# Performance work log

Measured on AMD Instinct MI355X. Metric: run time of the kernel, lower is better.

## Reference

```python
import jax, jax.numpy as jnp
import numpy as np

N_HEADS = 16
MAX_REL = 64  # max_relative_pos_len


def setup_inputs() -> dict:
    key = jax.random.key(0)
    ks = jax.random.split(key, 8)
    B, S, D = 2, 2048, 1024
    d = D // N_HEADS
    sc = 0.02
    return {
        "hidden_states": jax.random.normal(ks[0], (B, S, D), jnp.float32),
        "attention_mask": jnp.zeros((B, 1, 1, S), jnp.float32),
        "Wq": jax.random.normal(ks[1], (D, D), jnp.float32) * sc,
        "bq": jnp.zeros((D,), jnp.float32),
        "Wk": jax.random.normal(ks[2], (D, D), jnp.float32) * sc,
        "bk": jnp.zeros((D,), jnp.float32),
        "Wv": jax.random.normal(ks[3], (D, D), jnp.float32) * sc,
        "bv": jnp.zeros((D,), jnp.float32),
        "emb_k": jax.random.normal(ks[4], (2 * MAX_REL + 1, d), jnp.float32) * sc,
        "emb_v": jax.random.normal(ks[5], (2 * MAX_REL + 1, d), jnp.float32) * sc,
    }


def reference(hidden_states, attention_mask, Wq, bq, Wk, bk, Wv, bv, emb_k, emb_v):
    B, S, D = hidden_states.shape
    H = N_HEADS
    d = D // H
    scale = 1.0 / jnp.sqrt(jnp.asarray(d, hidden_states.dtype))

    def heads(x):  # [B,S,D] -> [B,H,S,d]
        return x.reshape(B, S, H, d).transpose(0, 2, 1, 3)

    q = heads(hidden_states @ Wq + bq)
    k = heads(hidden_states @ Wk + bk)
    v = heads(hidden_states @ Wv + bv)

    # relative position indices, clamped: [S_q, S_k]
    rel_idx = jnp.clip(jnp.arange(S)[:, None] - jnp.arange(S)[None, :], -MAX_REL, MAX_REL) + MAX_REL
    rel_k = emb_k[rel_idx]  # [S, S, d]

    # content scores + relative-key bias, both scaled by 1/sqrt(d)
    scores = (jnp.einsum('bhqd,bhkd->bhqk', q, k)
              + jnp.einsum('bhqd,qkd->bhqk', q, rel_k)) * scale
    scores = scores + attention_mask
    probs = jax.nn.softmax(scores, axis=-1)  # dropout is identity at p=0

    rel_v = emb_v[rel_idx]  # [S, S, d]
    ctx = (jnp.einsum('bhqk,bhkd->bhqd', probs, v)
           + jnp.einsum('bhqk,qkd->bhqd', probs, rel_v))
    return ctx.transpose(0, 2, 1, 3).reshape(B, S, D)
```

## Files before the change

kernel.cpp:

```cpp
#include <hip/hip_runtime.h>
#include <stdint.h>

typedef unsigned short u16;
typedef __attribute__((ext_vector_type(8))) short short8;
typedef __attribute__((ext_vector_type(4))) float f32x4;
typedef __attribute__((ext_vector_type(4))) unsigned short u16x4;

#define S_LEN 2048
#define NH 16
#define DMODEL 1024
#define NR 129
#define LOG2E 1.44269504f

#define MFMA(a,b,c) __builtin_amdgcn_mfma_f32_16x16x32_bf16((a),(b),(c),0,0,0)

__device__ __forceinline__ u16 f2bf(float f){
  uint32_t u = __float_as_uint(f);
  u += 0x7fff + ((u >> 16) & 1);
  return (u16)(u >> 16);
}
__device__ __forceinline__ float bf2f(u16 h){ return __uint_as_float(((uint32_t)h) << 16); }

__device__ __forceinline__ uint32_t cvtpk(float lo, float hi){
  uint32_t r;
  asm("v_cvt_pk_bf16_f32 %0, %1, %2" : "=v"(r) : "v"(lo), "v"(hi));
  return r;
}

__device__ __forceinline__ void gl_lds16(const u16* g, u16* l){
  __builtin_amdgcn_global_load_lds((const __attribute__((address_space(1))) void*)g,
                                   (__attribute__((address_space(3))) void*)l, 16, 0, 0);
}

__global__ __launch_bounds__(256) void k_prep(const float* __restrict__ X,
                                              const float* __restrict__ Wq, const float* __restrict__ Wk,
                                              const float* __restrict__ Wv, const float* __restrict__ Wemb,
                                              const float* __restrict__ mask,
                                              u16* __restrict__ Xb, u16* __restrict__ Wt,
                                              u16* __restrict__ Eb, float* __restrict__ maskL){
  const int bid = blockIdx.x, tid = threadIdx.x;
  if (bid < 4096){
    int i = bid * 256 + tid;
    const float4* xp = (const float4*)X;
    float4 v = xp[i];
    u16x4 o; o.x = f2bf(v.x); o.y = f2bf(v.y); o.z = f2bf(v.z); o.w = f2bf(v.w);
    *(u16x4*)(Xb + (size_t)i * 4) = o;
  } else if (bid < 4864){
    int b2 = bid - 4096;
    int z = b2 >> 8;
    const float* W = (z == 0) ? Wq : (z == 1) ? Wk : Wv;
    u16* Ot = Wt + (size_t)z * 1024 * 1024;
    __shared__ float t[64][65];
    int k0 = ((b2 >> 4) & 15) * 64, n0 = (b2 & 15) * 64;
    int c = tid & 63, r0 = (tid >> 6) * 16;
    #pragma unroll
    for (int i = 0; i < 16; ++i) t[r0 + i][c] = W[(size_t)(k0 + r0 + i) * 1024 + n0 + c];
    __syncthreads();
    #pragma unroll
    for (int i = 0; i < 16; ++i) Ot[(size_t)(n0 + r0 + i) * 1024 + k0 + c] = f2bf(t[c][r0 + i]);
  } else if (bid < 4900){
    int idx = (bid - 4864) * 256 + tid;
    if (idx < 144 * 64){
      int r = idx >> 6;
      Eb[idx] = (r < NR) ? f2bf(Wemb[idx]) : (u16)0;
    }
  } else {
    int idx = (bid - 4900) * 256 + tid;
    maskL[idx] = mask[idx] * LOG2E;
  }
}

__global__ __launch_bounds__(256) void k_qkv(const u16* __restrict__ Xb, const u16* __restrict__ Wt,
                                             const float* __restrict__ bq, const float* __restrict__ bk,
                                             const float* __restrict__ bv,
                                             u16* __restrict__ Qs, u16* __restrict__ Kb, u16* __restrict__ Vp){
  const int z = blockIdx.z;
  const u16* W = Wt + (size_t)z * 1024 * 1024;
  const float* bias = (z == 0) ? bq : (z == 1) ? bk : bv;
  const float vs = (z == 0) ? 0.125f * LOG2E : 1.0f;
  const int n0 = blockIdx.x * 128, m0 = blockIdx.y * 128;
  const int tid = threadIdx.x, w = tid >> 6, lane = tid & 63, l15 = lane & 15, quad = lane >> 4;
  const int wm = (w >> 1) * 64, wn = (w & 1) * 64;
  __shared__ __attribute__((aligned(16))) u16 As[128 * 32];
  __shared__ __attribute__((aligned(16))) u16 Bs[128 * 32];
  __shared__ __attribute__((aligned(16))) u16 Ts[64][136];
  f32x4 acc[4][4];
  #pragma unroll
  for (int i = 0; i < 4; ++i)
    #pragma unroll
    for (int j = 0; j < 4; ++j) acc[i][j] = (f32x4){0.f,0.f,0.f,0.f};

  const int rA = lane >> 2, cA = (lane & 3) * 8;
  const u16* aBase = Xb + (size_t)(m0 + w * 16 + rA) * 1024 + cA;
  const u16* bBase = W  + (size_t)(n0 + w * 16 + rA) * 1024 + cA;
  u16* aDst0 = As + (w * 16) * 32;  u16* aDst1 = As + (64 + w * 16) * 32;
  u16* bDst0 = Bs + (w * 16) * 32;  u16* bDst1 = Bs + (64 + w * 16) * 32;

  if (z == 2){
    for (int k0 = 0; k0 < 1024; k0 += 32){
      __syncthreads();
      gl_lds16(aBase + k0,             aDst0);
      gl_lds16(aBase + 64 * 1024 + k0, aDst1);
      gl_lds16(bBase + k0,             bDst0);
      gl_lds16(bBase + 64 * 1024 + k0, bDst1);
      __syncthreads();
      short8 af[4], bfr[4];
      #pragma unroll
      for (int f = 0; f < 4; ++f){
        af[f]  = *(const short8*)(As + (wm + f * 16 + l15) * 32 + quad * 8);
        bfr[f] = *(const short8*)(Bs + (wn + f * 16 + l15) * 32 + quad * 8);
      }
      #pragma unroll
      for (int i = 0; i < 4; ++i)
        #pragma unroll
        for (int j = 0; j < 4; ++j) acc[i][j] = MFMA(af[i], bfr[j], acc[i][j]);
    }
    const int hn0 = n0 >> 6;
    const int bb = m0 >> 11, sb = m0 & 2047;
    #pragma unroll
    for (int h2 = 0; h2 < 2; ++h2){
      __syncthreads();
      if ((w & 1) == h2){
        #pragma unroll
        for (int i = 0; i < 4; ++i){
          int sl0 = (w >> 1) * 64 + i * 16 + quad * 4;
          #pragma unroll
          for (int j = 0; j < 4; ++j){
            int d = j * 16 + l15;
            float bsv = bias[n0 + h2 * 64 + d];
            u16x4 vv;
            #pragma unroll
            for (int r = 0; r < 4; ++r) vv[r] = f2bf(acc[i][j][r] + bsv);
            *(u16x4*)&Ts[d][sl0] = vv;
          }
        }
      }
      __syncthreads();
      size_t gbase = ((size_t)(bb * 16 + hn0 + h2) * 64) * S_LEN + sb;
      #pragma unroll
      for (int it = 0; it < 4; ++it){
        int c2 = tid + it * 256;
        int d = c2 >> 4, m = c2 & 15;
        int blk = (m >> 3) * 64, mb = m & 7;
        int q = mb >> 1, f = (mb & 1) * 2;
        const u16* lo = &Ts[d][blk + f * 16 + q * 4];
        const u16* hi = &Ts[d][blk + (f + 1) * 16 + q * 4];
        short8 vv;
        #pragma unroll
        for (int u = 0; u < 4; ++u){ vv[u] = (short)lo[u]; vv[4 + u] = (short)hi[u]; }
        *(short8*)(Vp + gbase + (size_t)d * S_LEN + blk + mb * 8) = vv;
      }
    }
  } else {
    for (int k0 = 0; k0 < 1024; k0 += 32){
      __syncthreads();
      gl_lds16(aBase + k0,             aDst0);
      gl_lds16(aBase + 64 * 1024 + k0, aDst1);
      gl_lds16(bBase + k0,             bDst0);
      gl_lds16(bBase + 64 * 1024 + k0, bDst1);
      __syncthreads();
      short8 af[4], bfr[4];
      #pragma unroll
      for (int f = 0; f < 4; ++f){
        af[f]  = *(const short8*)(As + (wm + f * 16 + l15) * 32 + quad * 8);
        bfr[f] = *(const short8*)(Bs + (wn + f * 16 + l15) * 32 + quad * 8);
      }
      #pragma unroll
      for (int i = 0; i < 4; ++i)
        #pragma unroll
        for (int j = 0; j < 4; ++j) acc[i][j] = MFMA(bfr[j], af[i], acc[i][j]);
    }
    u16* outp = (z == 0) ? Qs : Kb;
    #pragma unroll
    for (int i = 0; i < 4; ++i){
      int srow = m0 + wm + i * 16 + l15;
      int bb = srow >> 11, s = srow & 2047;
      #pragma unroll
      for (int j = 0; j < 4; ++j){
        int coln = n0 + wn + j * 16 + quad * 4;
        f32x4 bsv4 = *(const f32x4*)&bias[coln];
        int hh = coln >> 6, jd = coln & 63;
        u16x4 ov;
        #pragma unroll
        for (int r = 0; r < 4; ++r) ov[r] = f2bf((acc[i][j][r] + bsv4[r]) * vs);
        *(u16x4*)(outp + (((size_t)(bb * 16 + hh)) * S_LEN + s) * 64 + jd) = ov;
      }
    }
  }
}

__global__ __launch_bounds__(256, 3) void k_flash(const u16* __restrict__ QS, const u16* __restrict__ KB,
                                                  const u16* __restrict__ VP, const u16* __restrict__ EMBK,
                                                  const float* __restrict__ maskL, const float* __restrict__ embv,
                                                  float* __restrict__ out){
  const int g = blockIdx.y; const int b = g >> 4; const int h = g & 15;
  const int q0 = blockIdx.x * 64;
  const int tid = threadIdx.x;
  const int w = tid >> 6; const int lane = tid & 63;
  const int l15 = lane & 15; const int quad = lane >> 4;
  const int wm = w * 16;
  const int rqb = quad * 4;
  const int qrow = q0 + wm + l15;

  __shared__ union UKE {
    struct {
      __attribute__((aligned(16))) u16 K[2][4096];
      __attribute__((aligned(16))) u16 V[2][4096];
    } s;
    struct {
      __attribute__((aligned(16))) u16 Psb[64][128];
      __attribute__((aligned(16))) u16 Evs[64][128];
    } t;
  } uu;
  __shared__ __attribute__((aligned(16))) u16 QEb[4][16][128];

  const int lrow = lane >> 3;
  const int lsw  = ((lane & 7) ^ lrow) * 8;
  const u16* kS = KB + ((size_t)g * S_LEN + w * 16 + lrow) * 64 + lsw;
  const u16* vS = VP + ((size_t)(g * 64 + w * 16 + lrow)) * S_LEN + lsw;
  const float* mBase = maskL + b * S_LEN;

  {
    u16* kd = uu.s.K[0] + (w * 16) * 64;
    u16* vd = uu.s.V[0] + (w * 16) * 64;
    gl_lds16(kS,             kd);
    gl_lds16(kS + 8 * 64,    kd + 512);
    gl_lds16(vS,             vd);
    gl_lds16(vS + 8 * S_LEN, vd + 512);
  }

  f32x4 mcur[4];
  #pragma unroll
  for (int fn = 0; fn < 4; ++fn) mcur[fn] = *(const f32x4*)(mBase + fn * 16 + rqb);

  const u16* qptr = QS + ((size_t)g * S_LEN + q0 + wm + l15) * 64 + quad * 8;
  short8 qa0 = *(const short8*)qptr;
  short8 qa1 = *(const short8*)(qptr + 32);

  float qeLf = 0.f;
  #pragma unroll
  for (int fn = 0; fn < 9; ++fn){
    const u16* ep = EMBK + (fn * 16 + l15) * 64 + quad * 8;
    short8 eb0 = *(const short8*)ep;
    short8 eb1 = *(const short8*)(ep + 32);
    f32x4 c = (f32x4){0.f,0.f,0.f,0.f};
    c = MFMA(qa0, eb0, c);
    c = MFMA(qa1, eb1, c);
    if (fn < 8){
      #pragma unroll
      for (int r = 0; r < 4; ++r) QEb[w][rqb + r][fn * 16 + l15] = f2bf(c[r]);
    } else {
      int srcl = (l15 >> 2) << 4;
      float t0 = __shfl(c[0], srcl, 64);
      float t1 = __shfl(c[1], srcl, 64);
      float t2 = __shfl(c[2], srcl, 64);
      float t3 = __shfl(c[3], srcl, 64);
      int rr = l15 & 3;
      float qv = (rr == 0) ? t0 : (rr == 1) ? t1 : (rr == 2) ? t2 : t3;
      qeLf = bf2f(f2bf(qv));
    }
  }
  __syncthreads();

  const float qeR = bf2f(QEb[w][l15][0]);
  const float qeL = qeLf;

  short8 bones;
  {
    short one = (l15 == 0) ? (short)0x3F80 : (short)0;
    #pragma unroll
    for (int j = 0; j < 8; ++j) bones[j] = one;
  }

  const int rsw = l15 & 7;
  const int kO0 = ((quad     ^ rsw) * 8);
  const int kO1 = (((quad+4) ^ rsw) * 8);
  const int vO0 = (((quad*2)     ^ rsw) * 8);
  const int vO1 = (((quad*2 + 1) ^ rsw) * 8);

  f32x4 o[4];
  #pragma unroll
  for (int f = 0; f < 4; ++f) o[f] = (f32x4){0.f,0.f,0.f,0.f};
  f32x4 lacc = (f32x4){0.f,0.f,0.f,0.f};
  float ll0v[4] = {0.f,0.f,0.f,0.f};
  float ll_mx = 0.f;
  float rsb_s = 0.f;
  uint32_t st0[8] = {0,0,0,0,0,0,0,0};
  uint32_t st1[8] = {0,0,0,0,0,0,0,0};
  uint32_t st2[8] = {0,0,0,0,0,0,0,0};

  int cur = 0;
  for (int kt = 0; kt < S_LEN; kt += 64){
    const int ktn = kt + 64;

    if (ktn < S_LEN){
      u16* kd = uu.s.K[cur ^ 1] + (w * 16) * 64;
      u16* vd = uu.s.V[cur ^ 1] + (w * 16) * 64;
      gl_lds16(kS + (size_t)ktn * 64,       kd);
      gl_lds16(kS + (size_t)(ktn + 8) * 64, kd + 512);
      gl_lds16(vS + ktn,                    vd);
      gl_lds16(vS + ktn + 8 * S_LEN,        vd + 512);
    }

    const bool leftC  = (kt <= q0 - 128);
    const bool rightC = (kt >= q0 + 128);
    const float qeadd = leftC ? qeL : (rightC ? qeR : 0.f);

    const u16* ks = uu.s.K[cur];
    f32x4 p4[4];
    __builtin_amdgcn_s_setprio(1);
    #pragma unroll
    for (int fn = 0; fn < 4; ++fn){
      const u16* krow = ks + (fn * 16 + l15) * 64;
      short8 kb0 = *(const short8*)(krow + kO0);
      short8 kb1 = *(const short8*)(krow + kO1);
      f32x4 c = mcur[fn] + qeadd;
      c = MFMA(kb0, qa0, c);
      c = MFMA(kb1, qa1, c);
      p4[fn] = c;
    }
    __builtin_amdgcn_s_setprio(0);

    f32x4 mnext[4];
    if (ktn < S_LEN){
      #pragma unroll
      for (int fn = 0; fn < 4; ++fn) mnext[fn] = *(const f32x4*)(mBase + ktn + fn * 16 + rqb);
    }

    if (leftC | rightC){
      #pragma unroll
      for (int fn = 0; fn < 4; ++fn)
        #pragma unroll
        for (int r = 0; r < 4; ++r) p4[fn][r] = __builtin_amdgcn_exp2f(p4[fn][r]);
    } else {
      #pragma unroll
      for (int fn = 0; fn < 4; ++fn){
        int kbase = kt + fn * 16 + rqb;
        #pragma unroll
        for (int r = 0; r < 4; ++r){
          int dq = qrow - (kbase + r) + 64;
          int ridx = min(max(dq, 0), 127);
          float qv = (dq >= 128) ? qeL : bf2f(QEb[w][l15][ridx]);
          float p = __builtin_amdgcn_exp2f(p4[fn][r] + qv);
          ll_mx += (dq >= 128) ? p : 0.f;
          rsb_s += (dq >= 1 && dq <= 127) ? p : 0.f;
          p4[fn][r] = p;
        }
      }
    }

    __builtin_amdgcn_s_setprio(1);
    const u16* vsb = uu.s.V[cur];
    #pragma unroll
    for (int fp = 0; fp < 2; ++fp){
      union { uint32_t u[4]; short8 s8; } pk;
      pk.u[0] = cvtpk(p4[2 * fp][0],     p4[2 * fp][1]);
      pk.u[1] = cvtpk(p4[2 * fp][2],     p4[2 * fp][3]);
      pk.u[2] = cvtpk(p4[2 * fp + 1][0], p4[2 * fp + 1][1]);
      pk.u[3] = cvtpk(p4[2 * fp + 1][2], p4[2 * fp + 1][3]);
      if (kt == q0 - 64){
        #pragma unroll
        for (int u4 = 0; u4 < 4; ++u4) st0[fp * 4 + u4] = pk.u[u4];
      } else if (kt == q0){
        #pragma unroll
        for (int u4 = 0; u4 < 4; ++u4) st1[fp * 4 + u4] = pk.u[u4];
      } else if (kt == q0 + 64){
        #pragma unroll
        for (int u4 = 0; u4 < 4; ++u4) st2[fp * 4 + u4] = pk.u[u4];
      }
      short8 pa = pk.s8;
      lacc = MFMA(pa, bones, lacc);
      const int vO = fp ? vO1 : vO0;
      #pragma unroll
      for (int fd = 0; fd < 4; ++fd){
        short8 vb = *(const short8*)(vsb + (fd * 16 + l15) * 64 + vO);
        o[fd] = MFMA(pa, vb, o[fd]);
      }
    }
    __builtin_amdgcn_s_setprio(0);

    if (kt == q0 - 128){
      #pragma unroll
      for (int r = 0; r < 4; ++r) ll0v[r] = lacc[r];
    }
    if (ktn < S_LEN){
      #pragma unroll
      for (int fn = 0; fn < 4; ++fn) mcur[fn] = mnext[fn];
    }
    __syncthreads();
    cur ^= 1;
  }

  {
    short8 z8 = (short8){0,0,0,0,0,0,0,0};
    #pragma unroll
    for (int i = 0; i < 4; ++i) ((short8*)uu.t.Psb)[tid + i * 256] = z8;
    int d = tid & 63, t4 = tid >> 6;
    #pragma unroll
    for (int it = 0; it < 32; ++it){
      int t = t4 + it * 4;
      float v = (t <= 126) ? embv[(size_t)(127 - t) * 64 + d] : 0.f;
      uu.t.Evs[d][(((t >> 3) ^ (d & 7)) << 3) | (t & 7)] = f2bf(v);
    }
  }
  __syncthreads();

  auto bandw = [&](int ktb, const uint32_t* st){
    #pragma unroll
    for (int fn = 0; fn < 4; ++fn)
      #pragma unroll
      for (int r = 0; r < 4; ++r){
        int dq = qrow - (ktb + fn * 16 + rqb + r) + 64;
        if (dq >= 1 && dq <= 127){
          int t = 127 - dq;
          uu.t.Psb[wm + l15][(((t >> 3) ^ rsw) << 3) | (t & 7)] =
            (u16)(st[(fn >> 1) * 4 + (fn & 1) * 2 + (r >> 1)] >> ((r & 1) * 16));
        }
      }
  };
  if (q0 >= 64) bandw(q0 - 64, st0);
  bandw(q0, st1);
  if (q0 + 64 < S_LEN) bandw(q0 + 64, st2);
  __syncthreads();

  f32x4 ob[4];
  #pragma unroll
  for (int f = 0; f < 4; ++f) ob[f] = (f32x4){0.f,0.f,0.f,0.f};
  #pragma unroll
  for (int kb = 0; kb < 4; ++kb){
    const int go = ((kb * 4 + quad) ^ rsw) << 3;
    short8 pa = *(const short8*)&uu.t.Psb[wm + l15][go];
    #pragma unroll
    for (int fd = 0; fd < 4; ++fd){
      short8 vb = *(const short8*)&uu.t.Evs[fd * 16 + l15][go];
      ob[fd] = MFMA(pa, vb, ob[fd]);
    }
  }

  #pragma unroll
  for (int st = 16; st < 64; st <<= 1){
    ll_mx += __shfl_xor(ll_mx, st, 64);
    rsb_s += __shfl_xor(rsb_s, st, 64);
  }

  float inv[4], tl[4], trr[4];
  #pragma unroll
  for (int r = 0; r < 4; ++r){
    float L   = __shfl(lacc[r], quad << 4);
    float l0  = __shfl(ll0v[r], quad << 4);
    int src   = (quad << 4) + rqb + r;
    float lmx = __shfl(ll_mx, src);
    float rv  = __shfl(rsb_s, src);
    inv[r] = 1.f / L;
    tl[r]  = (l0 + lmx) * inv[r];
    trr[r] = 1.f - tl[r] - rv * inv[r];
  }

  #pragma unroll
  for (int fd = 0; fd < 4; ++fd){
    int dim = fd * 16 + l15;
    float evL = embv[(size_t)128 * 64 + dim];
    float evR = embv[dim];
    #pragma unroll
    for (int r = 0; r < 4; ++r){
      int row = q0 + wm + rqb + r;
      float val = (o[fd][r] + ob[fd][r]) * inv[r] + tl[r] * evL + trr[r] * evR;
      out[((size_t)(b * S_LEN + row)) * DMODEL + h * 64 + dim] = val;
    }
  }
}

extern "C" void kernel_launch(void* const* d_in, const int* in_sizes, int n_in,
                              void* d_out, int out_size, void* d_ws, size_t ws_size,
                              hipStream_t stream){
  const float* X    = (const float*)d_in[0];
  const float* mask = (const float*)d_in[1];
  const float* Wq   = (const float*)d_in[2];
  const float* bq   = (const float*)d_in[3];
  const float* Wk   = (const float*)d_in[4];
  const float* bk   = (const float*)d_in[5];
  const float* Wv   = (const float*)d_in[6];
  const float* bv   = (const float*)d_in[7];
  const float* embk = (const float*)d_in[8];
  const float* embv = (const float*)d_in[9];
  float* out = (float*)d_out;
  char* ws = (char*)d_ws;

  u16* XB   = (u16*)(ws + 0);
  u16* WT   = (u16*)(ws + 8388608);
  u16* EKB  = (u16*)(ws + 14680064);
  u16* QS   = (u16*)(ws + 14698496);
  u16* KB   = (u16*)(ws + 23087104);
  u16* VP   = (u16*)(ws + 31475712);
  float* MSL = (float*)(ws + 48252928);

  k_prep   <<<4916, 256, 0, stream>>>(X, Wq, Wk, Wv, embk, mask, XB, WT, EKB, MSL);
  k_qkv    <<<dim3(8, 32, 3), 256, 0, stream>>>(XB, WT, bq, bk, bv, QS, KB, VP);
  k_flash  <<<dim3(32, 32), 256, 0, stream>>>(QS, KB, VP, EKB, MSL, embv, out);
}
```

Baseline: 235.8 us.

## Double flash query tile to 128 rows with 8 waves sharing K/V tiles

Result: no change. 238.3 us (+1.1%).

```diff
diff --git a/kernel.cpp b/kernel.cpp
--- a/kernel.cpp
+++ b/kernel.cpp
@@ -189,45 +189,40 @@
   }
 }
 
-__global__ __launch_bounds__(256, 3) void k_flash(const u16* __restrict__ QS, const u16* __restrict__ KB,
+__global__ __launch_bounds__(512, 4) void k_flash(const u16* __restrict__ QS, const u16* __restrict__ KB,
                                                   const u16* __restrict__ VP, const u16* __restrict__ EMBK,
                                                   const float* __restrict__ maskL, const float* __restrict__ embv,
                                                   float* __restrict__ out){
   const int g = blockIdx.y; const int b = g >> 4; const int h = g & 15;
-  const int q0 = blockIdx.x * 64;
+  const int q0 = blockIdx.x * 128;
   const int tid = threadIdx.x;
   const int w = tid >> 6; const int lane = tid & 63;
   const int l15 = lane & 15; const int quad = lane >> 4;
   const int wm = w * 16;
   const int rqb = quad * 4;
   const int qrow = q0 + wm + l15;
-
-  __shared__ union UKE {
+  const int tb0 = (q0 + wm) & ~63;
+
+  __shared__ union U1 {
     struct {
       __attribute__((aligned(16))) u16 K[2][4096];
       __attribute__((aligned(16))) u16 V[2][4096];
     } s;
-    struct {
-      __attribute__((aligned(16))) u16 Psb[64][128];
-      __attribute__((aligned(16))) u16 Evs[64][128];
-    } t;
+    __attribute__((aligned(16))) u16 Psb[128][128];
   } uu;
-  __shared__ __attribute__((aligned(16))) u16 QEb[4][16][128];
+  __shared__ union U2 {
+    __attribute__((aligned(16))) u16 QEb[8][16][128];
+    __attribute__((aligned(16))) u16 Evs[64][128];
+  } qq;
 
   const int lrow = lane >> 3;
   const int lsw  = ((lane & 7) ^ lrow) * 8;
-  const u16* kS = KB + ((size_t)g * S_LEN + w * 16 + lrow) * 64 + lsw;
-  const u16* vS = VP + ((size_t)(g * 64 + w * 16 + lrow)) * S_LEN + lsw;
+  const u16* kS = KB + ((size_t)g * S_LEN + w * 8 + lrow) * 64 + lsw;
+  const u16* vS = VP + ((size_t)(g * 64 + w * 8 + lrow)) * S_LEN + lsw;
   const float* mBase = maskL + b * S_LEN;
 
-  {
-    u16* kd = uu.s.K[0] + (w * 16) * 64;
-    u16* vd = uu.s.V[0] + (w * 16) * 64;
-    gl_lds16(kS,             kd);
-    gl_lds16(kS + 8 * 64,    kd + 512);
-    gl_lds16(vS,             vd);
-    gl_lds16(vS + 8 * S_LEN, vd + 512);
-  }
+  gl_lds16(kS, uu.s.K[0] + (w * 8) * 64);
+  gl_lds16(vS, uu.s.V[0] + (w * 8) * 64);
 
   f32x4 mcur[4];
   #pragma unroll
@@ -248,7 +243,7 @@
     c = MFMA(qa1, eb1, c);
     if (fn < 8){
       #pragma unroll
-      for (int r = 0; r < 4; ++r) QEb[w][rqb + r][fn * 16 + l15] = f2bf(c[r]);
+      for (int r = 0; r < 4; ++r) qq.QEb[w][rqb + r][fn * 16 + l15] = f2bf(c[r]);
     } else {
       int srcl = (l15 >> 2) << 4;
       float t0 = __shfl(c[0], srcl, 64);
@@ -262,7 +257,7 @@
   }
   __syncthreads();
 
-  const float qeR = bf2f(QEb[w][l15][0]);
+  const float qeR = bf2f(qq.QEb[w][l15][0]);
   const float qeL = qeLf;
 
   short8 bones;
@@ -294,16 +289,12 @@
     const int ktn = kt + 64;
 
     if (ktn < S_LEN){
-      u16* kd = uu.s.K[cur ^ 1] + (w * 16) * 64;
-      u16* vd = uu.s.V[cur ^ 1] + (w * 16) * 64;
-      gl_lds16(kS + (size_t)ktn * 64,       kd);
-      gl_lds16(kS + (size_t)(ktn + 8) * 64, kd + 512);
-      gl_lds16(vS + ktn,                    vd);
-      gl_lds16(vS + ktn + 8 * S_LEN,        vd + 512);
-    }
-
-    const bool leftC  = (kt <= q0 - 128);
-    const bool rightC = (kt >= q0 + 128);
+      gl_lds16(kS + (size_t)ktn * 64, uu.s.K[cur ^ 1] + (w * 8) * 64);
+      gl_lds16(vS + ktn,              uu.s.V[cur ^ 1] + (w * 8) * 64);
+    }
+
+    const bool leftC  = (kt <= tb0 - 128);
+    const bool rightC = (kt >= tb0 + 128);
     const float qeadd = leftC ? qeL : (rightC ? qeR : 0.f);
 
     const u16* ks = uu.s.K[cur];
@@ -340,7 +331,7 @@
         for (int r = 0; r < 4; ++r){
           int dq = qrow - (kbase + r) + 64;
           int ridx = min(max(dq, 0), 127);
-          float qv = (dq >= 128) ? qeL : bf2f(QEb[w][l15][ridx]);
+          float qv = (dq >= 128) ? qeL : bf2f(qq.QEb[w][l15][ridx]);
           float p = __builtin_amdgcn_exp2f(p4[fn][r] + qv);
           ll_mx += (dq >= 128) ? p : 0.f;
           rsb_s += (dq >= 1 && dq <= 127) ? p : 0.f;
@@ -358,13 +349,13 @@
       pk.u[1] = cvtpk(p4[2 * fp][2],     p4[2 * fp][3]);
       pk.u[2] = cvtpk(p4[2 * fp + 1][0], p4[2 * fp + 1][1]);
       pk.u[3] = cvtpk(p4[2 * fp + 1][2], p4[2 * fp + 1][3]);
-      if (kt == q0 - 64){
+      if (kt == tb0 - 64){
         #pragma unroll
         for (int u4 = 0; u4 < 4; ++u4) st0[fp * 4 + u4] = pk.u[u4];
-      } else if (kt == q0){
+      } else if (kt == tb0){
         #pragma unroll
         for (int u4 = 0; u4 < 4; ++u4) st1[fp * 4 + u4] = pk.u[u4];
-      } else if (kt == q0 + 64){
+      } else if (kt == tb0 + 64){
         #pragma unroll
         for (int u4 = 0; u4 < 4; ++u4) st2[fp * 4 + u4] = pk.u[u4];
       }
@@ -379,7 +370,7 @@
     }
     __builtin_amdgcn_s_setprio(0);
 
-    if (kt == q0 - 128){
+    if (kt == tb0 - 128){
       #pragma unroll
       for (int r = 0; r < 4; ++r) ll0v[r] = lacc[r];
     }
@@ -394,13 +385,13 @@
   {
     short8 z8 = (short8){0,0,0,0,0,0,0,0};
     #pragma unroll
-    for (int i = 0; i < 4; ++i) ((short8*)uu.t.Psb)[tid + i * 256] = z8;
+    for (int i = 0; i < 4; ++i) ((short8*)uu.Psb)[tid + i * 512] = z8;
     int d = tid & 63, t4 = tid >> 6;
     #pragma unroll
-    for (int it = 0; it < 32; ++it){
-      int t = t4 + it * 4;
+    for (int it = 0; it < 16; ++it){
+      int t = t4 + it * 8;
       float v = (t <= 126) ? embv[(size_t)(127 - t) * 64 + d] : 0.f;
-      uu.t.Evs[d][(((t >> 3) ^ (d & 7)) << 3) | (t & 7)] = f2bf(v);
+      qq.Evs[d][(((t >> 3) ^ (d & 7)) << 3) | (t & 7)] = f2bf(v);
     }
   }
   __syncthreads();
@@ -413,14 +404,14 @@
         int dq = qrow - (ktb + fn * 16 + rqb + r) + 64;
         if (dq >= 1 && dq <= 127){
           int t = 127 - dq;
-          uu.t.Psb[wm + l15][(((t >> 3) ^ rsw) << 3) | (t & 7)] =
+          uu.Psb[wm + l15][(((t >> 3) ^ rsw) << 3) | (t & 7)] =
             (u16)(st[(fn >> 1) * 4 + (fn & 1) * 2 + (r >> 1)] >> ((r & 1) * 16));
         }
       }
   };
-  if (q0 >= 64) bandw(q0 - 64, st0);
-  bandw(q0, st1);
-  if (q0 + 64 < S_LEN) bandw(q0 + 64, st2);
+  if (tb0 >= 64) bandw(tb0 - 64, st0);
+  bandw(tb0, st1);
+  if (tb0 + 64 < S_LEN) bandw(tb0 + 64, st2);
   __syncthreads();
 
   f32x4 ob[4];
@@ -429,10 +420,10 @@
   #pragma unroll
   for (int kb = 0; kb < 4; ++kb){
     const int go = ((kb * 4 + quad) ^ rsw) << 3;
-    short8 pa = *(const short8*)&uu.t.Psb[wm + l15][go];
+    short8 pa = *(const short8*)&uu.Psb[wm + l15][go];
     #pragma unroll
     for (int fd = 0; fd < 4; ++fd){
-      short8 vb = *(const short8*)&uu.t.Evs[fd * 16 + l15][go];
+      short8 vb = *(const short8*)&qq.Evs[fd * 16 + l15][go];
       ob[fd] = MFMA(pa, vb, ob[fd]);
     }
   }
@@ -496,5 +487,5 @@
 
   k_prep   <<<4916, 256, 0, stream>>>(X, Wq, Wk, Wv, embk, mask, XB, WT, EKB, MSL);
   k_qkv    <<<dim3(8, 32, 3), 256, 0, stream>>>(XB, WT, bq, bk, bv, QS, KB, VP);
-  k_flash  <<<dim3(32, 32), 256, 0, stream>>>(QS, KB, VP, EKB, MSL, embv, out);
-}
+  k_flash  <<<dim3(16, 32), 512, 0, stream>>>(QS, KB, VP, EKB, MSL, embv, out);
+}
```

## Single-buffer K/V tiles and alias LDS to raise occupancy to five blocks

Applied to the files above, without the earlier changes.

Measured after the change: 262.9 us. +11.5%, slower.

```diff
diff --git a/kernel.cpp b/kernel.cpp
--- a/kernel.cpp
+++ b/kernel.cpp
@@ -189,7 +189,7 @@
   }
 }
 
-__global__ __launch_bounds__(256, 3) void k_flash(const u16* __restrict__ QS, const u16* __restrict__ KB,
+__global__ __launch_bounds__(256, 5) void k_flash(const u16* __restrict__ QS, const u16* __restrict__ KB,
                                                   const u16* __restrict__ VP, const u16* __restrict__ EMBK,
                                                   const float* __restrict__ maskL, const float* __restrict__ embv,
                                                   float* __restrict__ out){
@@ -202,17 +202,17 @@
   const int rqb = quad * 4;
   const int qrow = q0 + wm + l15;
 
-  __shared__ union UKE {
+  __shared__ union U1 {
     struct {
-      __attribute__((aligned(16))) u16 K[2][4096];
-      __attribute__((aligned(16))) u16 V[2][4096];
+      __attribute__((aligned(16))) u16 K[4096];
+      __attribute__((aligned(16))) u16 V[4096];
     } s;
-    struct {
-      __attribute__((aligned(16))) u16 Psb[64][128];
-      __attribute__((aligned(16))) u16 Evs[64][128];
-    } t;
+    __attribute__((aligned(16))) u16 Psb[64][128];
   } uu;
-  __shared__ __attribute__((aligned(16))) u16 QEb[4][16][128];
+  __shared__ union U2 {
+    __attribute__((aligned(16))) u16 QEb[4][16][128];
+    __attribute__((aligned(16))) u16 Evs[64][128];
+  } qq;
 
   const int lrow = lane >> 3;
   const int lsw  = ((lane & 7) ^ lrow) * 8;
@@ -221,8 +221,8 @@
   const float* mBase = maskL + b * S_LEN;
 
   {
-    u16* kd = uu.s.K[0] + (w * 16) * 64;
-    u16* vd = uu.s.V[0] + (w * 16) * 64;
+    u16* kd = uu.s.K + (w * 16) * 64;
+    u16* vd = uu.s.V + (w * 16) * 64;
     gl_lds16(kS,             kd);
     gl_lds16(kS + 8 * 64,    kd + 512);
     gl_lds16(vS,             vd);
@@ -248,7 +248,7 @@
     c = MFMA(qa1, eb1, c);
     if (fn < 8){
       #pragma unroll
-      for (int r = 0; r < 4; ++r) QEb[w][rqb + r][fn * 16 + l15] = f2bf(c[r]);
+      for (int r = 0; r < 4; ++r) qq.QEb[w][rqb + r][fn * 16 + l15] = f2bf(c[r]);
     } else {
       int srcl = (l15 >> 2) << 4;
       float t0 = __shfl(c[0], srcl, 64);
@@ -262,7 +262,7 @@
   }
   __syncthreads();
 
-  const float qeR = bf2f(QEb[w][l15][0]);
+  const float qeR = bf2f(qq.QEb[w][l15][0]);
   const float qeL = qeLf;
 
   short8 bones;
@@ -289,24 +289,14 @@
   uint32_t st1[8] = {0,0,0,0,0,0,0,0};
   uint32_t st2[8] = {0,0,0,0,0,0,0,0};
 
-  int cur = 0;
   for (int kt = 0; kt < S_LEN; kt += 64){
     const int ktn = kt + 64;
-
-    if (ktn < S_LEN){
-      u16* kd = uu.s.K[cur ^ 1] + (w * 16) * 64;
-      u16* vd = uu.s.V[cur ^ 1] + (w * 16) * 64;
-      gl_lds16(kS + (size_t)ktn * 64,       kd);
-      gl_lds16(kS + (size_t)(ktn + 8) * 64, kd + 512);
-      gl_lds16(vS + ktn,                    vd);
-      gl_lds16(vS + ktn + 8 * S_LEN,        vd + 512);
-    }
 
     const bool leftC  = (kt <= q0 - 128);
     const bool rightC = (kt >= q0 + 128);
     const float qeadd = leftC ? qeL : (rightC ? qeR : 0.f);
 
-    const u16* ks = uu.s.K[cur];
+    const u16* ks = uu.s.K;
     f32x4 p4[4];
     __builtin_amdgcn_s_setprio(1);
     #pragma unroll
@@ -340,7 +330,7 @@
         for (int r = 0; r < 4; ++r){
           int dq = qrow - (kbase + r) + 64;
           int ridx = min(max(dq, 0), 127);
-          float qv = (dq >= 128) ? qeL : bf2f(QEb[w][l15][ridx]);
+          float qv = (dq >= 128) ? qeL : bf2f(qq.QEb[w][l15][ridx]);
           float p = __builtin_amdgcn_exp2f(p4[fn][r] + qv);
           ll_mx += (dq >= 128) ? p : 0.f;
           rsb_s += (dq >= 1 && dq <= 127) ? p : 0.f;
@@ -350,7 +340,7 @@
     }
 
     __builtin_amdgcn_s_setprio(1);
-    const u16* vsb = uu.s.V[cur];
+    const u16* vsb = uu.s.V;
     #pragma unroll
     for (int fp = 0; fp < 2; ++fp){
       union { uint32_t u[4]; short8 s8; } pk;
@@ -386,21 +376,28 @@
     if (ktn < S_LEN){
       #pragma unroll
       for (int fn = 0; fn < 4; ++fn) mcur[fn] = mnext[fn];
-    }
-    __syncthreads();
-    cur ^= 1;
-  }
-
+      __syncthreads();
+      u16* kd = uu.s.K + (w * 16) * 64;
+      u16* vd = uu.s.V + (w * 16) * 64;
+      gl_lds16(kS + (size_t)ktn * 64,       kd);
+      gl_lds16(kS + (size_t)(ktn + 8) * 64, kd + 512);
+      gl_lds16(vS + ktn,                    vd);
+      gl_lds16(vS + ktn + 8 * S_LEN,        vd + 512);
+      __syncthreads();
+    }
+  }
+
+  __syncthreads();
   {
     short8 z8 = (short8){0,0,0,0,0,0,0,0};
     #pragma unroll
-    for (int i = 0; i < 4; ++i) ((short8*)uu.t.Psb)[tid + i * 256] = z8;
+    for (int i = 0; i < 4; ++i) ((short8*)uu.Psb)[tid + i * 256] = z8;
     int d = tid & 63, t4 = tid >> 6;
     #pragma unroll
     for (int it = 0; it < 32; ++it){
       int t = t4 + it * 4;
       float v = (t <= 126) ? embv[(size_t)(127 - t) * 64 + d] : 0.f;
-      uu.t.Evs[d][(((t >> 3) ^ (d & 7)) << 3) | (t & 7)] = f2bf(v);
+      qq.Evs[d][(((t >> 3) ^ (d & 7)) << 3) | (t & 7)] = f2bf(v);
     }
   }
   __syncthreads();
@@ -413,7 +410,7 @@
         int dq = qrow - (ktb + fn * 16 + rqb + r) + 64;
         if (dq >= 1 && dq <= 127){
           int t = 127 - dq;
-          uu.t.Psb[wm + l15][(((t >> 3) ^ rsw) << 3) | (t & 7)] =
+          uu.Psb[wm + l15][(((t >> 3) ^ rsw) << 3) | (t & 7)] =
             (u16)(st[(fn >> 1) * 4 + (fn & 1) * 2 + (r >> 1)] >> ((r & 1) * 16));
         }
       }
@@ -429,10 +426,10 @@
   #pragma unroll
   for (int kb = 0; kb < 4; ++kb){
     const int go = ((kb * 4 + quad) ^ rsw) << 3;
-    short8 pa = *(const short8*)&uu.t.Psb[wm + l15][go];
+    short8 pa = *(const short8*)&uu.Psb[wm + l15][go];
     #pragma unroll
     for (int fd = 0; fd < 4; ++fd){
-      short8 vb = *(const short8*)&uu.t.Evs[fd * 16 + l15][go];
+      short8 vb = *(const short8*)&qq.Evs[fd * 16 + l15][go];
       ob[fd] = MFMA(pa, vb, ob[fd]);
     }
   }
```
